# Performance work log

Measured on AMD Instinct MI355X. Metric: run time of the kernel, lower is better.

Reference implementation:

```python
import jax, jax.numpy as jnp
import numpy as np

NUM_CAMS = 1
NUM_HEADS = 1
NUM_LEVELS = 1
NUM_POINTS = 4
NUM_DEPTH = 128
EMBED = 128  # must equal NUM_DEPTH (output_proj is applied to the depth axis)


def setup_inputs() -> dict:
    key0 = jax.random.key(0)
    ks = jax.random.split(key0, 12)
    bsv, nq, nv = 1, 1024, 1024  # nq == nv == H*W (32*32)
    off_dim = NUM_CAMS * NUM_HEADS * NUM_LEVELS * NUM_DEPTH * NUM_POINTS * 2  # 1024
    aw_dim = NUM_CAMS * NUM_HEADS * NUM_LEVELS * NUM_DEPTH * NUM_POINTS       # 512
    return {
        "query": jax.random.normal(ks[0], (bsv, nq, EMBED), jnp.float32),
        "key": jax.random.normal(ks[1], (NUM_CAMS, nv, bsv, EMBED), jnp.float32),
        "value": jax.random.normal(ks[2], (NUM_CAMS, nv, bsv, EMBED), jnp.float32),
        "ref_3d": jax.random.uniform(ks[3], (bsv * NUM_CAMS, nq * NUM_DEPTH, 2), jnp.float32),
        "spatial_shapes": jnp.array([[32, 32]], dtype=jnp.int32),
        "W_off": jax.random.normal(ks[4], (EMBED, off_dim), jnp.float32) * 0.02,
        "b_off": jax.random.normal(ks[5], (off_dim,), jnp.float32) * 0.02,
        "W_attn": jax.random.normal(ks[6], (EMBED, aw_dim), jnp.float32) * 0.02,
        "b_attn": jax.random.normal(ks[7], (aw_dim,), jnp.float32) * 0.02,
        "W_v": jax.random.normal(ks[8], (EMBED, EMBED), jnp.float32) / np.sqrt(EMBED),
        "b_v": jnp.zeros((EMBED,), jnp.float32),
        "W_o": jax.random.normal(ks[9], (EMBED, EMBED), jnp.float32) / np.sqrt(EMBED),
        "b_o": jnp.zeros((EMBED,), jnp.float32),
    }


def _bilinear_sample(val, H, W, x, y):
    """grid_sample(align_corners=False, padding=zeros) equivalent.
    val: [B, H*W, D]; x, y: [B, Q, P] in pixel coords. Returns [B, Q, P, D]."""
    B, Q, P = x.shape
    D = val.shape[-1]
    x0f = jnp.floor(x); y0f = jnp.floor(y)
    ix0 = x0f.astype(jnp.int32); iy0 = y0f.astype(jnp.int32)
    wx1 = x - x0f; wy1 = y - y0f
    wx0 = 1.0 - wx1; wy0 = 1.0 - wy1

    def corner(ix, iy, w):
        valid = (ix >= 0) & (ix < W) & (iy >= 0) & (iy < H)
        idx = jnp.clip(iy, 0, H - 1) * W + jnp.clip(ix, 0, W - 1)  # [B,Q,P]
        g = jnp.take_along_axis(val, idx.reshape(B, Q * P)[:, :, None], axis=1)
        g = g.reshape(B, Q, P, D)
        return g * (w * valid.astype(val.dtype))[..., None]

    return (corner(ix0, iy0, wx0 * wy0)
            + corner(ix0 + 1, iy0, wx1 * wy0)
            + corner(ix0, iy0 + 1, wx0 * wy1)
            + corner(ix0 + 1, iy0 + 1, wx1 * wy1))


def reference(query, key, value, ref_3d, spatial_shapes,
              W_off, b_off, W_attn, b_attn, W_v, b_v, W_o, b_o):
    bsv, nq, E = query.shape
    cams, nv, bs, _ = key.shape
    identity = query

    # key/value: [cams, nv, bs, E] -> [bsv, nv, E]
    key2 = jnp.transpose(key, (2, 0, 1, 3)).reshape(bsv, nv, E)
    val = jnp.flip(value, axis=0)
    val = jnp.transpose(val, (2, 0, 1, 3)).reshape(bsv, nv, E)
    val = val @ W_v + b_v
    val = val.reshape(bsv * cams, nv, E)  # num_heads=1 -> head_dim=E

    # offsets / attention weights (heads=levels=1 axes squeezed)
    off = (query @ W_off + b_off).reshape(bsv, nq, cams, NUM_DEPTH, NUM_POINTS, 2)
    aw = (query @ W_attn + b_attn).reshape(bsv, nq, cams, NUM_DEPTH, NUM_LEVELS * NUM_POINTS)
    aw = jax.nn.softmax(aw, axis=-1).reshape(bsv, nq, cams, NUM_DEPTH, NUM_POINTS)
    off = jnp.transpose(off, (0, 2, 1, 3, 4, 5)).reshape(bsv * cams, nq * NUM_DEPTH, NUM_POINTS, 2)
    aw = jnp.transpose(aw, (0, 2, 1, 3, 4)).reshape(bsv * cams, nq * NUM_DEPTH, NUM_POINTS)

    H = spatial_shapes[0, 0]
    W = spatial_shapes[0, 1]
    norm = jnp.stack([W, H]).astype(off.dtype)  # [W, H]
    loc = ref_3d[:, :, None, :] + off / norm    # [B, Qe, P, 2] in [0,1]
    x = loc[..., 0] * W.astype(loc.dtype) - 0.5
    y = loc[..., 1] * H.astype(loc.dtype) - 0.5

    sampled = _bilinear_sample(val, H, W, x, y)          # [B, Qe, P, E]
    out = jnp.einsum('bqpe,bqp->bqe', sampled, aw)       # weighted sum over points

    out = out.reshape(bsv, cams, nq, NUM_DEPTH, E).mean(axis=1)  # [bsv, nq, depth, E]
    out = (out * key2[:, :, None, :]).mean(axis=-1)              # [bsv, nq, depth]
    out = out @ W_o + b_o                                        # depth == EMBED
    return out + identity  # dropout = identity in eval
```

## Files before the change

kernel.cpp:

```cpp
#include <hip/hip_runtime.h>
#include <hip/hip_bf16.h>


#define NQ   1024
#define NV   1024
#define ND   128
#define NP   4
#define IMG_W 32
#define IMG_H 32

__device__ __forceinline__ void gemm_tile64(
    const float* __restrict__ A,
    const float* __restrict__ B,
    int N, bool nt,
    const float* __restrict__ bias,
    const float* __restrict__ cvec,
    float* __restrict__ C,
    int m0, int n0, float* sA, float* sB) {
  const int tid = threadIdx.x;

#pragma unroll
  for (int k = 0; k < 8; ++k) {
    int c = tid + k * 256;
    int m = c & 63, e4 = c >> 6;
    const float4 v = *(const float4*)(A + (size_t)(m0 + m) * 128 + e4 * 4);
    sA[(e4 * 4 + 0) * 64 + m] = v.x;
    sA[(e4 * 4 + 1) * 64 + m] = v.y;
    sA[(e4 * 4 + 2) * 64 + m] = v.z;
    sA[(e4 * 4 + 3) * 64 + m] = v.w;
  }
  if (nt) {
#pragma unroll
    for (int k = 0; k < 8; ++k) {
      int c = tid + k * 256;
      int n = c & 63, e4 = c >> 6;
      const float4 v = *(const float4*)(B + (size_t)(n0 + n) * 128 + e4 * 4);
      sB[(e4 * 4 + 0) * 64 + n] = v.x;
      sB[(e4 * 4 + 1) * 64 + n] = v.y;
      sB[(e4 * 4 + 2) * 64 + n] = v.z;
      sB[(e4 * 4 + 3) * 64 + n] = v.w;
    }
  } else {
#pragma unroll
    for (int k = 0; k < 8; ++k) {
      int c = tid + k * 256;
      int n4 = c & 15, e = c >> 4;
      *(float4*)(sB + e * 64 + n4 * 4) =
          *(const float4*)(B + (size_t)e * N + n0 + n4 * 4);
    }
  }
  __syncthreads();

  const int tx = tid & 15, ty = tid >> 4;
  float acc[4][4] = {};
#pragma unroll 8
  for (int e = 0; e < 128; ++e) {
    const float4 a = *(const float4*)(sA + e * 64 + ty * 4);
    const float4 b = *(const float4*)(sB + e * 64 + tx * 4);
    acc[0][0] += a.x * b.x; acc[0][1] += a.x * b.y; acc[0][2] += a.x * b.z; acc[0][3] += a.x * b.w;
    acc[1][0] += a.y * b.x; acc[1][1] += a.y * b.y; acc[1][2] += a.y * b.z; acc[1][3] += a.y * b.w;
    acc[2][0] += a.z * b.x; acc[2][1] += a.z * b.y; acc[2][2] += a.z * b.z; acc[2][3] += a.z * b.w;
    acc[3][0] += a.w * b.x; acc[3][1] += a.w * b.y; acc[3][2] += a.w * b.z; acc[3][3] += a.w * b.w;
  }

  float4 bv = make_float4(0.f, 0.f, 0.f, 0.f);
  if (bias) bv = *(const float4*)(bias + n0 + tx * 4);
#pragma unroll
  for (int i = 0; i < 4; ++i) {
    const int m = m0 + ty * 4 + i;
    float cv = cvec ? cvec[m] : 0.f;
    float4 r;
    r.x = acc[i][0] + bv.x + cv;
    r.y = acc[i][1] + bv.y + cv;
    r.z = acc[i][2] + bv.z + cv;
    r.w = acc[i][3] + bv.w + cv;
    *(float4*)(C + (size_t)m * N + n0 + tx * 4) = r;
  }
}

__global__ __launch_bounds__(256, 2) void p1_kernel(
    const float* __restrict__ query, const float* __restrict__ key,
    const float* __restrict__ W_off, const float* __restrict__ b_off,
    const float* __restrict__ W_attn, const float* __restrict__ b_attn,
    const float* __restrict__ W_v, const float* __restrict__ b_v,
    float* __restrict__ off_ws, float* __restrict__ aw_ws,
    float* __restrict__ keyp_ws, float* __restrict__ c_ws) {
  __shared__ float sA[128 * 64];
  __shared__ float sB[128 * 64];
  const int t = blockIdx.x;
  if (t < 256) {
    gemm_tile64(query, W_off, 1024, false, b_off, nullptr, off_ws,
                (t >> 4) * 64, (t & 15) * 64, sA, sB);
  } else if (t < 384) {
    const int u = t - 256;
    gemm_tile64(query, W_attn, 512, false, b_attn, nullptr, aw_ws,
                (u >> 3) * 64, (u & 7) * 64, sA, sB);
  } else if (t < 416) {
    const int u = t - 384;
    gemm_tile64(key, W_v, 128, true, nullptr, nullptr, keyp_ws,
                (u >> 1) * 64, (u & 1) * 64, sA, sB);
  } else {
    for (int i = 0; i < 4; ++i) {
      const int q = threadIdx.x + i * 256;
      float s = 0.f;
      for (int e = 0; e < 128; ++e) s += key[(size_t)q * 128 + e] * b_v[e];
      c_ws[q] = s;
    }
  }
}

__global__ __launch_bounds__(256, 2) void p2_kernel(
    const float* __restrict__ keyp_ws, const float* __restrict__ value,
    const float* __restrict__ c_ws, float* __restrict__ dotv_ws) {
  __shared__ float sA[128 * 64];
  __shared__ float sB[128 * 64];
  const int t = blockIdx.x;
  gemm_tile64(keyp_ws, value, 1024, true, nullptr, c_ws, dotv_ws,
              (t >> 4) * 64, (t & 15) * 64, sA, sB);
}

__global__ __launch_bounds__(256) void p3_kernel(
    const float* __restrict__ dotv,
    const float* __restrict__ off,
    const float* __restrict__ awr,
    const float* __restrict__ ref3d,
    const float* __restrict__ query,
    const float* __restrict__ W_o,
    const float* __restrict__ b_o,
    float* __restrict__ out) {
  __shared__ float img[2][NV];
  __shared__ float o1s[2][ND];

  const int tid = threadIdx.x;
  const int q0 = blockIdx.x * 2;

#pragma unroll
  for (int k = 0; k < 2; ++k) {
    int c = tid + k * 256;
    int qq = c >> 8, v4 = c & 255;
    *(float4*)(&img[qq][v4 * 4]) =
        *(const float4*)(dotv + (size_t)(q0 + qq) * NV + v4 * 4);
  }
  __syncthreads();

  {
    const int qq = tid >> 7;
    const int q = q0 + qq;
    const int d = tid & 127;
    const float* im = img[qq];
    const size_t qe = (size_t)q * ND + d;

    const float rx = ref3d[qe * 2 + 0];
    const float ry = ref3d[qe * 2 + 1];

    const float* awp = awr + (size_t)q * (ND * NP) + d * NP;
    const float a0 = awp[0], a1 = awp[1], a2 = awp[2], a3 = awp[3];
    const float mx = fmaxf(fmaxf(a0, a1), fmaxf(a2, a3));
    const float e0 = __expf(a0 - mx), e1 = __expf(a1 - mx),
                e2 = __expf(a2 - mx), e3 = __expf(a3 - mx);
    const float inv = 1.0f / (e0 + e1 + e2 + e3);
    const float w[4] = {e0 * inv, e1 * inv, e2 * inv, e3 * inv};

    const float* op = off + (size_t)q * (ND * NP * 2) + d * (NP * 2);

    float acc = 0.0f;
#pragma unroll
    for (int p = 0; p < NP; ++p) {
      const float x = rx * (float)IMG_W + op[p * 2 + 0] - 0.5f;
      const float y = ry * (float)IMG_H + op[p * 2 + 1] - 0.5f;
      const float xf = floorf(x), yf = floorf(y);
      const int ix0 = (int)xf, iy0 = (int)yf;
      const float wx1 = x - xf, wy1 = y - yf;
      const float wx0 = 1.0f - wx1, wy0 = 1.0f - wy1;

      float s = 0.0f;
#pragma unroll
      for (int cy = 0; cy < 2; ++cy) {
#pragma unroll
        for (int cx = 0; cx < 2; ++cx) {
          const int ix = ix0 + cx, iy = iy0 + cy;
          const bool valid = (ix >= 0) & (ix < IMG_W) & (iy >= 0) & (iy < IMG_H);
          const int cix = min(max(ix, 0), IMG_W - 1);
          const int ciy = min(max(iy, 0), IMG_H - 1);
          const float wgt = (cx ? wx1 : wx0) * (cy ? wy1 : wy0);
          s += valid ? im[ciy * IMG_W + cix] * wgt : 0.0f;
        }
      }
      acc += w[p] * s;
    }
    o1s[qq][d] = acc * (1.0f / 128.0f);
  }
  __syncthreads();

  {
    const int qq = tid >> 7;
    const int q = q0 + qq;
    const int n = tid & 127;
    float acc = b_o[n] + query[(size_t)q * 128 + n];
#pragma unroll 8
    for (int d = 0; d < 128; ++d)
      acc += o1s[qq][d] * W_o[(size_t)d * 128 + n];
    out[(size_t)q * 128 + n] = acc;
  }
}

extern "C" void kernel_launch(void* const* d_in, const int* in_sizes, int n_in,
                              void* d_out, int out_size, void* d_ws, size_t ws_size,
                              hipStream_t stream) {
  const float* query  = (const float*)d_in[0];
  const float* key    = (const float*)d_in[1];
  const float* value  = (const float*)d_in[2];
  const float* ref3d  = (const float*)d_in[3];
  const float* W_off  = (const float*)d_in[5];
  const float* b_off  = (const float*)d_in[6];
  const float* W_attn = (const float*)d_in[7];
  const float* b_attn = (const float*)d_in[8];
  const float* W_v    = (const float*)d_in[9];
  const float* b_v    = (const float*)d_in[10];
  const float* W_o    = (const float*)d_in[11];
  const float* b_o    = (const float*)d_in[12];
  float* out = (float*)d_out;

  float* ws = (float*)d_ws;
  float* off_ws  = ws;
  float* aw_ws   = off_ws + (size_t)NQ * 1024;
  float* keyp_ws = aw_ws + (size_t)NQ * 512;
  float* c_ws    = keyp_ws + (size_t)NQ * 128;
  float* dotv_ws = c_ws + 1024;

  p1_kernel<<<417, 256, 0, stream>>>(query, key, W_off, b_off, W_attn, b_attn,
                                     W_v, b_v, off_ws, aw_ws, keyp_ws, c_ws);
  p2_kernel<<<256, 256, 0, stream>>>(keyp_ws, value, c_ws, dotv_ws);
  p3_kernel<<<512, 256, 0, stream>>>(dotv_ws, off_ws, aw_ws, ref3d, query,
                                     W_o, b_o, out);
}
```

Baseline: 113.7 us.

## Move projection and value-dot GEMMs to bf16 MFMA tiles with restaged kernels

Replaces the scalar fp32 64x64 GEMM tiles for the offset, attention-weight and key-value dot products with 128x128 tiles that convert inputs to bf16 in swizzled LDS and use 16x16x32 bf16 MFMA instructions. A new first kernel transposes W_off and W_attn into the workspace and computes the key projection, so all three large GEMMs run in one second kernel. The aim is to cut FP32 ALU time by using matrix cores. In exchange, inputs are rounded to bf16, which lowers accuracy of the offsets and dot products, and there is an extra transpose pass.

```diff
diff --git a/kernel.cpp b/kernel.cpp
--- a/kernel.cpp
+++ b/kernel.cpp
@@ -1,5 +1,4 @@
 #include <hip/hip_runtime.h>
-#include <hip/hip_bf16.h>
 
 
 #define NQ   1024
@@ -9,16 +8,20 @@
 #define IMG_W 32
 #define IMG_H 32
 
+typedef __attribute__((ext_vector_type(8))) short bfx8;
+typedef __attribute__((ext_vector_type(4))) float f32x4;
+
+__device__ __forceinline__ unsigned short bf_rne(float f) {
+  unsigned u = __float_as_uint(f);
+  return (unsigned short)((u + 0x7FFFu + ((u >> 16) & 1u)) >> 16);
+}
+
 __device__ __forceinline__ void gemm_tile64(
-    const float* __restrict__ A,
-    const float* __restrict__ B,
+    const float* __restrict__ A, const float* __restrict__ B,
     int N, bool nt,
-    const float* __restrict__ bias,
-    const float* __restrict__ cvec,
-    float* __restrict__ C,
-    int m0, int n0, float* sA, float* sB) {
+    const float* __restrict__ bias, const float* __restrict__ cvec,
+    float* __restrict__ C, int m0, int n0, float* sA, float* sB) {
   const int tid = threadIdx.x;
-
 #pragma unroll
   for (int k = 0; k < 8; ++k) {
     int c = tid + k * 256;
@@ -74,31 +77,54 @@
     r.y = acc[i][1] + bv.y + cv;
     r.z = acc[i][2] + bv.z + cv;
     r.w = acc[i][3] + bv.w + cv;
-    *(float4*)(C + (size_t)m * N + n0 + tx * 4) = r;
-  }
-}
-
-__global__ __launch_bounds__(256, 2) void p1_kernel(
-    const float* __restrict__ query, const float* __restrict__ key,
-    const float* __restrict__ W_off, const float* __restrict__ b_off,
-    const float* __restrict__ W_attn, const float* __restrict__ b_attn,
-    const float* __restrict__ W_v, const float* __restrict__ b_v,
-    float* __restrict__ off_ws, float* __restrict__ aw_ws,
-    float* __restrict__ keyp_ws, float* __restrict__ c_ws) {
-  __shared__ float sA[128 * 64];
-  __shared__ float sB[128 * 64];
+    *(float4*)(C + (size_t)m * 128 + n0 + tx * 4) = r;
+  }
+}
+
+__device__ __forceinline__ void transpose64(const float* __restrict__ src, int N,
+                                            int n0, float* __restrict__ dst,
+                                            float* lds) {
+  const int tid = threadIdx.x;
+#pragma unroll
+  for (int it = 0; it < 8; ++it) {
+    int c = tid + it * 256;
+    int k = c >> 4, cf = c & 15;
+    float4 v = *(const float4*)(src + (size_t)k * N + n0 + cf * 4);
+    lds[k * 65 + cf * 4 + 0] = v.x;
+    lds[k * 65 + cf * 4 + 1] = v.y;
+    lds[k * 65 + cf * 4 + 2] = v.z;
+    lds[k * 65 + cf * 4 + 3] = v.w;
+  }
+  __syncthreads();
+#pragma unroll
+  for (int it = 0; it < 8; ++it) {
+    int c = tid + it * 256;
+    int dn = c >> 5, kq = c & 31;
+    float4 v;
+    v.x = lds[(kq * 4 + 0) * 65 + dn];
+    v.y = lds[(kq * 4 + 1) * 65 + dn];
+    v.z = lds[(kq * 4 + 2) * 65 + dn];
+    v.w = lds[(kq * 4 + 3) * 65 + dn];
+    *(float4*)(dst + (size_t)(n0 + dn) * 128 + kq * 4) = v;
+  }
+}
+
+__global__ __launch_bounds__(256, 2) void d1_kernel(
+    const float* __restrict__ key, const float* __restrict__ W_v,
+    const float* __restrict__ b_v, const float* __restrict__ W_off,
+    const float* __restrict__ W_attn,
+    float* __restrict__ keyp_ws, float* __restrict__ c_ws,
+    float* __restrict__ wofft, float* __restrict__ wattnt) {
+  __shared__ float smem[16384];
   const int t = blockIdx.x;
-  if (t < 256) {
-    gemm_tile64(query, W_off, 1024, false, b_off, nullptr, off_ws,
-                (t >> 4) * 64, (t & 15) * 64, sA, sB);
-  } else if (t < 384) {
-    const int u = t - 256;
-    gemm_tile64(query, W_attn, 512, false, b_attn, nullptr, aw_ws,
-                (u >> 3) * 64, (u & 7) * 64, sA, sB);
-  } else if (t < 416) {
-    const int u = t - 384;
+  if (t < 16) {
+    transpose64(W_off, 1024, t * 64, wofft, smem);
+  } else if (t < 24) {
+    transpose64(W_attn, 512, (t - 16) * 64, wattnt, smem);
+  } else if (t < 56) {
+    const int u = t - 24;
     gemm_tile64(key, W_v, 128, true, nullptr, nullptr, keyp_ws,
-                (u >> 1) * 64, (u & 1) * 64, sA, sB);
+                (u >> 1) * 64, (u & 1) * 64, smem, smem + 8192);
   } else {
     for (int i = 0; i < 4; ++i) {
       const int q = threadIdx.x + i * 256;
@@ -109,25 +135,131 @@
   }
 }
 
-__global__ __launch_bounds__(256, 2) void p2_kernel(
-    const float* __restrict__ keyp_ws, const float* __restrict__ value,
-    const float* __restrict__ c_ws, float* __restrict__ dotv_ws) {
-  __shared__ float sA[128 * 64];
-  __shared__ float sB[128 * 64];
+__device__ __forceinline__ void mfma_tile128(
+    const float* __restrict__ A,
+    const float* __restrict__ B,
+    const float* __restrict__ bias,
+    const float* __restrict__ cvec,
+    float* __restrict__ C, int ldc,
+    int m0, int n0, unsigned short* sA, unsigned short* sB) {
+  const int tid = threadIdx.x;
+
+  {
+    const float* srcs[2] = {A, B};
+    const int r0s[2] = {m0, n0};
+    unsigned short* dsts[2] = {sA, sB};
+#pragma unroll
+    for (int s = 0; s < 2; ++s) {
+      const float* src = srcs[s];
+      const int r0 = r0s[s];
+      unsigned short* dst = dsts[s];
+#pragma unroll
+      for (int it = 0; it < 8; ++it) {
+        int c = tid + it * 256;
+        int r = c >> 4, cc = c & 15;
+        const float* p = src + (size_t)(r0 + r) * 128 + cc * 8;
+        float4 f0 = *(const float4*)p;
+        float4 f1 = *(const float4*)(p + 4);
+        bfx8 v;
+        v[0] = (short)bf_rne(f0.x); v[1] = (short)bf_rne(f0.y);
+        v[2] = (short)bf_rne(f0.z); v[3] = (short)bf_rne(f0.w);
+        v[4] = (short)bf_rne(f1.x); v[5] = (short)bf_rne(f1.y);
+        v[6] = (short)bf_rne(f1.z); v[7] = (short)bf_rne(f1.w);
+        int byte = r * 256 + ((cc * 16) ^ ((r & 15) << 4));
+        *(bfx8*)((char*)dst + byte) = v;
+      }
+    }
+  }
+  __syncthreads();
+
+  const int l = tid & 63;
+  const int w = tid >> 6;
+  const int wr = w >> 1, wc = w & 1;
+  const int lr = l & 15, g = l >> 4;
+
+  f32x4 acc[4][4];
+#pragma unroll
+  for (int mi = 0; mi < 4; ++mi)
+#pragma unroll
+    for (int ni = 0; ni < 4; ++ni) {
+      f32x4 z = {0.f, 0.f, 0.f, 0.f};
+      acc[mi][ni] = z;
+    }
+
+#pragma unroll
+  for (int ks = 0; ks < 4; ++ks) {
+    const int colb = (ks * 64 + g * 16) ^ (lr << 4);
+    bfx8 af[4], bfr[4];
+#pragma unroll
+    for (int mi = 0; mi < 4; ++mi) {
+      int r = wr * 64 + mi * 16 + lr;
+      af[mi] = *(const bfx8*)((const char*)sA + r * 256 + colb);
+    }
+#pragma unroll
+    for (int ni = 0; ni < 4; ++ni) {
+      int r = wc * 64 + ni * 16 + lr;
+      bfr[ni] = *(const bfx8*)((const char*)sB + r * 256 + colb);
+    }
+#pragma unroll
+    for (int mi = 0; mi < 4; ++mi)
+#pragma unroll
+      for (int ni = 0; ni < 4; ++ni)
+        acc[mi][ni] = __builtin_amdgcn_mfma_f32_16x16x32_bf16(
+            af[mi], bfr[ni], acc[mi][ni], 0, 0, 0);
+  }
+
+#pragma unroll
+  for (int mi = 0; mi < 4; ++mi) {
+    float cv[4];
+#pragma unroll
+    for (int i = 0; i < 4; ++i) {
+      int row = m0 + wr * 64 + mi * 16 + g * 4 + i;
+      cv[i] = cvec ? cvec[row] : 0.f;
+    }
+#pragma unroll
+    for (int ni = 0; ni < 4; ++ni) {
+      int col = n0 + wc * 64 + ni * 16 + lr;
+      float bn = bias ? bias[col] : 0.f;
+#pragma unroll
+      for (int i = 0; i < 4; ++i) {
+        int row = m0 + wr * 64 + mi * 16 + g * 4 + i;
+        C[(size_t)row * ldc + col] = acc[mi][ni][i] + bn + cv[i];
+      }
+    }
+  }
+}
+
+__global__ __launch_bounds__(256, 2) void d2_kernel(
+    const float* __restrict__ query, const float* __restrict__ keyp,
+    const float* __restrict__ value,
+    const float* __restrict__ wofft, const float* __restrict__ wattnt,
+    const float* __restrict__ b_off, const float* __restrict__ b_attn,
+    const float* __restrict__ c_ws,
+    float* __restrict__ off_ws, float* __restrict__ aw_ws,
+    float* __restrict__ dotv_ws) {
+  __shared__ __align__(16) unsigned short sAB[32768];
+  unsigned short* sA = sAB;
+  unsigned short* sB = sAB + 16384;
   const int t = blockIdx.x;
-  gemm_tile64(keyp_ws, value, 1024, true, nullptr, c_ws, dotv_ws,
-              (t >> 4) * 64, (t & 15) * 64, sA, sB);
+  if (t < 64) {
+    mfma_tile128(query, wofft, b_off, nullptr, off_ws, 1024,
+                 (t >> 3) * 128, (t & 7) * 128, sA, sB);
+  } else if (t < 96) {
+    const int u = t - 64;
+    mfma_tile128(query, wattnt, b_attn, nullptr, aw_ws, 512,
+                 (u >> 2) * 128, (u & 3) * 128, sA, sB);
+  } else {
+    const int u = t - 96;
+    mfma_tile128(keyp, value, nullptr, c_ws, dotv_ws, 1024,
+                 (u >> 3) * 128, (u & 7) * 128, sA, sB);
+  }
 }
 
 __global__ __launch_bounds__(256) void p3_kernel(
-    const float* __restrict__ dotv,
-    const float* __restrict__ off,
-    const float* __restrict__ awr,
-    const float* __restrict__ ref3d,
-    const float* __restrict__ query,
-    const float* __restrict__ W_o,
-    const float* __restrict__ b_o,
-    float* __restrict__ out) {
+    const float* __restrict__ dotv, const float* __restrict__ off,
+    const float* __restrict__ awr, const float* __restrict__ ref3d,
+    const float* __restrict__ query, const float* __restrict__ W_o,
+    const float* __restrict__ b_o, float* __restrict__ out) {
   __shared__ float img[2][NV];
   __shared__ float o1s[2][ND];
 
@@ -159,7 +291,7 @@
     const float e0 = __expf(a0 - mx), e1 = __expf(a1 - mx),
                 e2 = __expf(a2 - mx), e3 = __expf(a3 - mx);
     const float inv = 1.0f / (e0 + e1 + e2 + e3);
-    const float w[4] = {e0 * inv, e1 * inv, e2 * inv, e3 * inv};
+    const float wgt4[4] = {e0 * inv, e1 * inv, e2 * inv, e3 * inv};
 
     const float* op = off + (size_t)q * (ND * NP * 2) + d * (NP * 2);
 
@@ -186,7 +318,7 @@
           s += valid ? im[ciy * IMG_W + cix] * wgt : 0.0f;
         }
       }
-      acc += w[p] * s;
+      acc += wgt4[p] * s;
     }
     o1s[qq][d] = acc * (1.0f / 128.0f);
   }
@@ -227,10 +359,14 @@
   float* keyp_ws = aw_ws + (size_t)NQ * 512;
   float* c_ws    = keyp_ws + (size_t)NQ * 128;
   float* dotv_ws = c_ws + 1024;
-
-  p1_kernel<<<417, 256, 0, stream>>>(query, key, W_off, b_off, W_attn, b_attn,
-                                     W_v, b_v, off_ws, aw_ws, keyp_ws, c_ws);
-  p2_kernel<<<256, 256, 0, stream>>>(keyp_ws, value, c_ws, dotv_ws);
+  float* wofft   = dotv_ws + (size_t)NQ * 1024;
+  float* wattnt  = wofft + (size_t)1024 * 128;
+
+  d1_kernel<<<57, 256, 0, stream>>>(key, W_v, b_v, W_off, W_attn,
+                                    keyp_ws, c_ws, wofft, wattnt);
+  d2_kernel<<<160, 256, 0, stream>>>(query, keyp_ws, value, wofft, wattnt,
+                                     b_off, b_attn, c_ws,
+                                     off_ws, aw_ws, dotv_ws);
   p3_kernel<<<512, 256, 0, stream>>>(dotv_ws, off_ws, aw_ws, ref3d, query,
                                      W_o, b_o, out);
 }
```

Result: faster. 111.0 us (-2.4%).
